# Performance work log

Measured on AMD Instinct MI355X. Metric: run time of the kernel, lower is better.

The kernel has to match this reference:

```python
import jax, jax.numpy as jnp
import numpy as np

B, S, D = 4, 2048, 1024
H = 16
HD = D // H  # 64


def setup_inputs() -> dict:
    key = jax.random.key(0)
    kx, kq, kp = jax.random.split(key, 3)
    x = jax.random.normal(kx, (B, S, D), dtype=jnp.float32)
    # torch Linear weights are [out, in]; match init scale ~ U(-1/sqrt(in), 1/sqrt(in))
    lim = 1.0 / np.sqrt(D)
    w_qkv = jax.random.uniform(kq, (3 * D, D), dtype=jnp.float32, minval=-lim, maxval=lim)
    w_proj = jax.random.uniform(kp, (D, D), dtype=jnp.float32, minval=-lim, maxval=lim)
    return {"x": x, "w_qkv": w_qkv, "w_proj": w_proj}


def reference(x, w_qkv, w_proj):
    b, s, d = x.shape
    qkv = jnp.einsum('bsd,ed->bse', x, w_qkv)  # [B,S,3D]
    q, k, v = jnp.split(qkv, 3, axis=-1)
    # [B,H,S,HD]
    q = q.reshape(b, s, H, HD).transpose(0, 2, 1, 3)
    k = k.reshape(b, s, H, HD).transpose(0, 2, 1, 3)
    v = v.reshape(b, s, H, HD).transpose(0, 2, 1, 3)
    scale = 1.0 / np.sqrt(HD)
    attn = jnp.einsum('bhqd,bhkd->bhqk', q, k) * scale  # [B,H,S,S]
    causal = jnp.tril(jnp.ones((s, s), dtype=bool))
    attn = jnp.where(causal[None, None], attn, -jnp.inf)
    attn = jax.nn.softmax(attn, axis=-1)
    out = jnp.einsum('bhqk,bhkd->bhqd', attn, v)
    out = out.transpose(0, 2, 1, 3).reshape(b, s, d)
    return jnp.einsum('bsd,ed->bse', out, w_proj)
```

## Files before the change

### kernel.cpp

```cpp
#include <hip/hip_runtime.h>

typedef unsigned short u16;
typedef unsigned int u32;

#define B_ 4
#define S_ 2048
#define D_ 1024
#define H_ 16
#define HD_ 64
#define M_ (B_ * S_)
#define QK_ (2 * D_)

typedef __bf16 bf16x8 __attribute__((ext_vector_type(8)));
typedef float f32x4 __attribute__((ext_vector_type(4)));

#define MASKVAL (-1.0e30f)
#define RESCALE_THR 8.0f

static __device__ __forceinline__ u16 f2bf_hw(float f) {
    union { __bf16 b; u16 u; } v;
    v.b = (__bf16)f;
    return v.u;
}

static __device__ __forceinline__ void gload16(const u16* g, u16* l) {
    __builtin_amdgcn_global_load_lds(
        (const __attribute__((address_space(1))) void*)g,
        (__attribute__((address_space(3))) void*)l, 16, 0, 0);
}

__global__ __launch_bounds__(256) void cvt_bf16(const float* __restrict__ src,
                                                u16* __restrict__ dst) {
    size_t i = ((size_t)blockIdx.x * 256 + threadIdx.x) * 8;
    float4 a = *(const float4*)(src + i);
    float4 b = *(const float4*)(src + i + 4);
    union { u16 h[8]; int4 v; } pk;
    pk.h[0] = f2bf_hw(a.x); pk.h[1] = f2bf_hw(a.y);
    pk.h[2] = f2bf_hw(a.z); pk.h[3] = f2bf_hw(a.w);
    pk.h[4] = f2bf_hw(b.x); pk.h[5] = f2bf_hw(b.y);
    pk.h[6] = f2bf_hw(b.z); pk.h[7] = f2bf_hw(b.w);
    *(int4*)(dst + i) = pk.v;
}

template <int EPI>
__global__ __launch_bounds__(256) void gemm_bb(const u16* __restrict__ A,
                                               const u16* __restrict__ Bw,
                                               void* __restrict__ Cout,
                                               int Ndim, int Kdim) {
    __shared__ u16 Alds[128 * 64];
    __shared__ u16 Blds[128 * 64];
    const int t = threadIdx.x;
    const int bx = blockIdx.x, by = blockIdx.y;
    const int wave = t >> 6, lane = t & 63;
    const int ml = lane & 15, quad = lane >> 4;
    const int wm = (wave >> 1) * 64, wn = (wave & 1) * 64;
    const int rowA0 = by * 128, rowB0 = bx * 128;
    const int sr8 = lane >> 3;
    const int sc8 = (lane & 7) * 8;

    f32x4 acc[4][4];
    const f32x4 zero = {0.f, 0.f, 0.f, 0.f};
#pragma unroll
    for (int i = 0; i < 4; ++i)
#pragma unroll
        for (int j = 0; j < 4; ++j) acc[i][j] = zero;

    for (int k0 = 0; k0 < Kdim; k0 += 64) {
        __syncthreads();
#pragma unroll
        for (int p = 0; p < 4; ++p) {
            const int rbase = wave * 32 + p * 8;
            gload16(&A[(size_t)(rowA0 + rbase + sr8) * Kdim + k0 + sc8],
                    &Alds[rbase * 64]);
            gload16(&Bw[(size_t)(rowB0 + rbase + sr8) * Kdim + k0 + sc8],
                    &Blds[rbase * 64]);
        }
        __syncthreads();
#pragma unroll
        for (int kc = 0; kc < 2; ++kc) {
            bf16x8 a[4], b[4];
#pragma unroll
            for (int i = 0; i < 4; ++i)
                a[i] = *(const bf16x8*)(&Alds[(wm + i * 16 + ml) * 64 + kc * 32 + quad * 8]);
#pragma unroll
            for (int j = 0; j < 4; ++j)
                b[j] = *(const bf16x8*)(&Blds[(wn + j * 16 + ml) * 64 + kc * 32 + quad * 8]);
#pragma unroll
            for (int i = 0; i < 4; ++i)
#pragma unroll
                for (int j = 0; j < 4; ++j)
                    acc[i][j] = __builtin_amdgcn_mfma_f32_16x16x32_bf16(a[i], b[j], acc[i][j], 0, 0, 0);
        }
    }

    if constexpr (EPI == 0) {
        u16* C = (u16*)Cout;
#pragma unroll
        for (int i = 0; i < 4; ++i)
#pragma unroll
            for (int j = 0; j < 4; ++j)
#pragma unroll
                for (int r = 0; r < 4; ++r) {
                    int row = rowA0 + wm + i * 16 + quad * 4 + r;
                    int col = rowB0 + wn + j * 16 + ml;
                    C[(size_t)row * Ndim + col] = f2bf_hw(acc[i][j][r]);
                }
    } else if constexpr (EPI == 1) {
        u16* Vt = (u16*)Cout;
#pragma unroll
        for (int i = 0; i < 4; ++i)
#pragma unroll
            for (int j = 0; j < 4; ++j) {
                int row0 = rowA0 + wm + i * 16 + quad * 4;
                int col = rowB0 + wn + j * 16 + ml;
                int b = row0 >> 11;
                int s0 = row0 & (S_ - 1);
                union { u16 h[4]; ushort4 v; } pk;
#pragma unroll
                for (int r = 0; r < 4; ++r) pk.h[r] = f2bf_hw(acc[i][j][r]);
                *(ushort4*)(&Vt[((size_t)(b * D_ + col)) * S_ + s0]) = pk.v;
            }
    } else {
        float* C = (float*)Cout;
#pragma unroll
        for (int i = 0; i < 4; ++i)
#pragma unroll
            for (int j = 0; j < 4; ++j)
#pragma unroll
                for (int r = 0; r < 4; ++r) {
                    int row = rowA0 + wm + i * 16 + quad * 4 + r;
                    int col = rowB0 + wn + j * 16 + ml;
                    C[(size_t)row * Ndim + col] = acc[i][j][r];
                }
    }
}

__global__ __launch_bounds__(256, 3) void attn3(const u16* __restrict__ qk,
                                                const u16* __restrict__ Vt,
                                                u16* __restrict__ AO) {
    __shared__ u16 Klds[2][64 * 64];
    __shared__ u16 Vlds[2][64 * 64];
    __shared__ u32 Pw[4][32 * 32];
    const int t = threadIdx.x;
    const int wave = t >> 6, lane = t & 63;
    const int ml = lane & 15, quad = lane >> 4;

    const int jj = blockIdx.x >> 6;
    const int bh = blockIdx.x & 63;
    const int t4 = jj >> 2, r4 = jj & 3;
    const int j = (t4 < 2) ? (15 - 4 * t4 - r4) : (12 - 4 * t4 + r4);
    const int b = bh >> 4, h = bh & 15;
    const size_t rowbase = (size_t)b * S_;

    const int srow8 = lane >> 3;
    const int schunk = ((lane & 7) ^ srow8) * 8;

    const int qj0 = j * 128 + wave * 32;
    const int ktw = 2 * j + (wave >> 1);
    const int ktmax = 2 * j + 1;

    bf16x8 qf[2][2];
#pragma unroll
    for (int mi = 0; mi < 2; ++mi)
#pragma unroll
        for (int kc = 0; kc < 2; ++kc) {
            bf16x8 q = *(const bf16x8*)(&qk[(rowbase + qj0 + mi * 16 + ml) * QK_ +
                                            h * HD_ + kc * 32 + quad * 8]);
#pragma unroll
            for (int e = 0; e < 8; ++e) {
                float f = (float)q[e] * 0.125f;
                q[e] = (__bf16)f;
            }
            qf[mi][kc] = q;
        }

    f32x4 o[2][4];
    float m[2], ls[2];
    const f32x4 zero = {0.f, 0.f, 0.f, 0.f};
#pragma unroll
    for (int mi = 0; mi < 2; ++mi) {
#pragma unroll
        for (int nd = 0; nd < 4; ++nd) o[mi][nd] = zero;
        m[mi] = MASKVAL; ls[mi] = 0.f;
    }

    auto STAGE = [&](int buf, int kt) {
        const int kb = kt * 64;
#pragma unroll
        for (int p = 0; p < 2; ++p) {
            const int rbase = wave * 16 + p * 8;
            gload16(&qk[(rowbase + kb + rbase + srow8) * QK_ + D_ + h * HD_ + schunk],
                    &Klds[buf][rbase * 64]);
            gload16(&Vt[(size_t)(bh * HD_ + rbase + srow8) * S_ + kb + schunk],
                    &Vlds[buf][rbase * 64]);
        }
    };

    STAGE(0, 0);

    for (int kt = 0; kt <= ktmax; ++kt) {
        const int cur = kt & 1;
        if (kt < ktmax) {
            STAGE(cur ^ 1, kt + 1);
            asm volatile("s_waitcnt vmcnt(4)" ::: "memory");
        } else {
            asm volatile("s_waitcnt vmcnt(0)" ::: "memory");
        }
        __builtin_amdgcn_s_barrier();

        if (kt <= ktw) {
            const int kb = kt * 64;
            bf16x8 kf[4][2], vf[4][2];
#pragma unroll
            for (int ni = 0; ni < 4; ++ni)
#pragma unroll
                for (int kc = 0; kc < 2; ++kc) {
                    const int row = ni * 16 + ml;
                    const int sw = ((kc * 4 + quad) ^ (ml & 7)) * 8;
                    kf[ni][kc] = *(const bf16x8*)(&Klds[cur][row * 64 + sw]);
                    vf[ni][kc] = *(const bf16x8*)(&Vlds[cur][row * 64 + sw]);
                }

            f32x4 sc[2][4];
            __builtin_amdgcn_s_setprio(1);
#pragma unroll
            for (int mi = 0; mi < 2; ++mi)
#pragma unroll
                for (int ni = 0; ni < 4; ++ni) {
                    f32x4 s = zero;
#pragma unroll
                    for (int kc = 0; kc < 2; ++kc)
                        s = __builtin_amdgcn_mfma_f32_16x16x32_bf16(kf[ni][kc], qf[mi][kc], s, 0, 0, 0);
                    sc[mi][ni] = s;
                }
            __builtin_amdgcn_s_setprio(0);

            if (kb + 63 > qj0) {
#pragma unroll
                for (int mi = 0; mi < 2; ++mi) {
                    const int q = qj0 + mi * 16 + ml;
#pragma unroll
                    for (int ni = 0; ni < 4; ++ni)
#pragma unroll
                        for (int r = 0; r < 4; ++r) {
                            int k = kb + ni * 16 + quad * 4 + r;
                            if (k > q) sc[mi][ni][r] = MASKVAL;
                        }
                }
            }

#pragma unroll
            for (int mi = 0; mi < 2; ++mi) {
                float tm = sc[mi][0][0];
#pragma unroll
                for (int ni = 0; ni < 4; ++ni)
#pragma unroll
                    for (int r = 0; r < 4; ++r) tm = fmaxf(tm, sc[mi][ni][r]);
                tm = fmaxf(tm, __shfl_xor(tm, 16, 64));
                tm = fmaxf(tm, __shfl_xor(tm, 32, 64));
                if (__any(tm > m[mi] + RESCALE_THR)) {
                    float mn = fmaxf(m[mi], tm);
                    float al = __expf(m[mi] - mn);
                    m[mi] = mn;
                    ls[mi] *= al;
                    float alr[4];
#pragma unroll
                    for (int r = 0; r < 4; ++r)
                        alr[r] = __shfl(al, (lane & 48) + ((lane & 48) >> 2) + r, 64);
#pragma unroll
                    for (int nd = 0; nd < 4; ++nd)
#pragma unroll
                        for (int r = 0; r < 4; ++r) o[mi][nd][r] *= alr[r];
                }
                float sum = 0.f;
#pragma unroll
                for (int ni = 0; ni < 4; ++ni)
#pragma unroll
                    for (int r = 0; r < 4; ++r) {
                        float e = __expf(sc[mi][ni][r] - m[mi]);
                        sc[mi][ni][r] = e;
                        sum += e;
                    }
                ls[mi] += sum;
#pragma unroll
                for (int ni = 0; ni < 4; ++ni) {
                    union { u16 h[4]; ushort4 v; } pk;
#pragma unroll
                    for (int r = 0; r < 4; ++r) pk.h[r] = f2bf_hw(sc[mi][ni][r]);
                    const int row = mi * 16 + ml;
                    const int word = row * 32 +
                                     (((ni * 2 + (quad >> 1)) ^ (ml & 7)) << 2) +
                                     ((quad & 1) * 2);
                    *(ushort4*)(&Pw[wave][word]) = pk.v;
                }
            }
            asm volatile("s_waitcnt lgkmcnt(0)" ::: "memory");
            bf16x8 pf[2][2];
#pragma unroll
            for (int mi = 0; mi < 2; ++mi)
#pragma unroll
                for (int kc = 0; kc < 2; ++kc) {
                    const int row = mi * 16 + ml;
                    const int word = row * 32 + ((((kc * 4 + quad)) ^ (ml & 7)) << 2);
                    pf[mi][kc] = *(const bf16x8*)(&Pw[wave][word]);
                }
            __builtin_amdgcn_s_setprio(1);
#pragma unroll
            for (int mi = 0; mi < 2; ++mi)
#pragma unroll
                for (int nd = 0; nd < 4; ++nd)
#pragma unroll
                    for (int kc = 0; kc < 2; ++kc)
                        o[mi][nd] = __builtin_amdgcn_mfma_f32_16x16x32_bf16(pf[mi][kc], vf[nd][kc],
                                                                            o[mi][nd], 0, 0, 0);
            __builtin_amdgcn_s_setprio(0);
        }
        __builtin_amdgcn_s_barrier();
    }

#pragma unroll
    for (int mi = 0; mi < 2; ++mi) {
        float s = ls[mi];
        s += __shfl_xor(s, 16, 64);
        s += __shfl_xor(s, 32, 64);
        float rl = 1.0f / s;
        float rlr[4];
#pragma unroll
        for (int r = 0; r < 4; ++r)
            rlr[r] = __shfl(rl, (lane & 48) + ((lane & 48) >> 2) + r, 64);
#pragma unroll
        for (int nd = 0; nd < 4; ++nd)
#pragma unroll
            for (int r = 0; r < 4; ++r) {
                int srow = qj0 + mi * 16 + quad * 4 + r;
                AO[(rowbase + srow) * D_ + h * HD_ + nd * 16 + ml] =
                    f2bf_hw(o[mi][nd][r] * rlr[r]);
            }
    }
}

__global__ __launch_bounds__(256) void copy16(const int4* __restrict__ src,
                                              int4* __restrict__ dst) {
    size_t i = (size_t)blockIdx.x * 256 + threadIdx.x;
    dst[i] = src[i];
}

extern "C" void kernel_launch(void* const* d_in, const int* in_sizes, int n_in,
                              void* d_out, int out_size, void* d_ws, size_t ws_size,
                              hipStream_t stream) {
    const float* x = (const float*)d_in[0];
    const float* wqkv = (const float*)d_in[1];
    const float* wproj = (const float*)d_in[2];
    float* out = (float*)d_out;

    u16* qkw = (u16*)d_ws;
    u16* Vtw = qkw + (size_t)M_ * QK_;

    u16* xb = (u16*)d_out;
    u16* wprojb = xb + (size_t)M_ * D_;
    u16* wqkvb = wprojb + (size_t)D_ * D_;

    const size_t need = ((size_t)M_ * QK_ + 8388608  + (size_t)M_ * D_  +
                         (size_t)D_ * D_ ) * sizeof(u16);
    const bool bigws = ws_size >= need;
    u16* AOb    = bigws ? (Vtw + (size_t)8388608) : xb;
    u16* wprojd = bigws ? (AOb + (size_t)M_ * D_) : wprojb;
    u16* AOp    = bigws ? AOb : qkw;
    u16* wprojp = bigws ? wprojd : qkw + (size_t)M_ * D_;

    cvt_bf16<<<dim3(M_ * D_ / 2048), 256, 0, stream>>>(x, xb);
    cvt_bf16<<<dim3(D_ * D_ / 2048), 256, 0, stream>>>(wproj, wprojd);
    cvt_bf16<<<dim3(3 * D_ * D_ / 2048), 256, 0, stream>>>(wqkv, wqkvb);

    gemm_bb<0><<<dim3(QK_ / 128, M_ / 128), 256, 0, stream>>>(xb, wqkvb, qkw, QK_, D_);
    gemm_bb<1><<<dim3(D_ / 128, M_ / 128), 256, 0, stream>>>(
        xb, wqkvb + (size_t)QK_ * D_, Vtw, D_, D_);
    attn3<<<dim3(1024), 256, 0, stream>>>(qkw, Vtw, AOb);
    if (!bigws) {
        copy16<<<dim3((unsigned)(((size_t)M_ * D_ + (size_t)D_ * D_) * 2 / (256 * 16))),
                 256, 0, stream>>>((const int4*)AOb, (int4*)qkw);
    }
    gemm_bb<2><<<dim3(D_ / 128, M_ / 128), 256, 0, stream>>>(AOp, wprojp, out, D_, D_);
}
```

Before: 269.1 us.

## Merge QK and V projection GEMMs and defer PV MFMA to overlap next tile load

The separate QK and V projection GEMMs become one launch, with the epilogue choosing row-major or transposed V output by block column. In attention, the P·V product is deferred to the next iteration so it runs after the next K/V tile load is issued, overlapping MFMA work with memory latency. The P scratch buffer changes to a padded 72-element row layout with a simpler swizzle. K fragments are now loaded per column tile to reduce register pressure. V fragments persist across iterations, which raises register use and adds a tail PV call after the loop.

```diff
diff --git a/kernel.cpp b/kernel.cpp
--- a/kernel.cpp
+++ b/kernel.cpp
@@ -46,6 +46,7 @@
 __global__ __launch_bounds__(256) void gemm_bb(const u16* __restrict__ A,
                                                const u16* __restrict__ Bw,
                                                void* __restrict__ Cout,
+                                               void* __restrict__ C2,
                                                int Ndim, int Kdim) {
     __shared__ u16 Alds[128 * 64];
     __shared__ u16 Blds[128 * 64];
@@ -93,7 +94,8 @@
         }
     }
 
-    if constexpr (EPI == 0) {
+    const bool doVt = (EPI == 1) || (EPI == 3 && bx >= 16);
+    if ((EPI == 0) || (EPI == 3 && !doVt)) {
         u16* C = (u16*)Cout;
 #pragma unroll
         for (int i = 0; i < 4; ++i)
@@ -105,14 +107,15 @@
                     int col = rowB0 + wn + j * 16 + ml;
                     C[(size_t)row * Ndim + col] = f2bf_hw(acc[i][j][r]);
                 }
-    } else if constexpr (EPI == 1) {
-        u16* Vt = (u16*)Cout;
+    } else if (doVt) {
+        u16* Vt = (EPI == 3) ? (u16*)C2 : (u16*)Cout;
+        const int voff = (EPI == 3) ? 2048 : 0;
 #pragma unroll
         for (int i = 0; i < 4; ++i)
 #pragma unroll
             for (int j = 0; j < 4; ++j) {
                 int row0 = rowA0 + wm + i * 16 + quad * 4;
-                int col = rowB0 + wn + j * 16 + ml;
+                int col = rowB0 + wn + j * 16 + ml - voff;
                 int b = row0 >> 11;
                 int s0 = row0 & (S_ - 1);
                 union { u16 h[4]; ushort4 v; } pk;
@@ -140,10 +143,11 @@
                                                 u16* __restrict__ AO) {
     __shared__ u16 Klds[2][64 * 64];
     __shared__ u16 Vlds[2][64 * 64];
-    __shared__ u32 Pw[4][32 * 32];
+    __shared__ u16 Pw[4][32 * 72];
     const int t = threadIdx.x;
     const int wave = t >> 6, lane = t & 63;
     const int ml = lane & 15, quad = lane >> 4;
+    const int mhx = (ml & 8) >> 1;
 
     const int jj = blockIdx.x >> 6;
     const int bh = blockIdx.x & 63;
@@ -159,6 +163,8 @@
     const int ktw = 2 * j + (wave >> 1);
     const int ktmax = 2 * j + 1;
 
+    u16* pwb = &Pw[wave][0];
+
     bf16x8 qf[2][2];
 #pragma unroll
     for (int mi = 0; mi < 2; ++mi)
@@ -183,6 +189,8 @@
         for (int nd = 0; nd < 4; ++nd) o[mi][nd] = zero;
         m[mi] = MASKVAL; ls[mi] = 0.f;
     }
+
+    bf16x8 vf[4][2];
 
     auto STAGE = [&](int buf, int kt) {
         const int kb = kt * 64;
@@ -196,12 +204,35 @@
         }
     };
 
+    auto PV = [&]() {
+        bf16x8 pf[2][2];
+#pragma unroll
+        for (int mi = 0; mi < 2; ++mi)
+#pragma unroll
+            for (int kc = 0; kc < 2; ++kc)
+                pf[mi][kc] = *(const bf16x8*)(&pwb[(mi * 16 + ml) * 72 +
+                                                   (((kc * 4 + quad) ^ mhx) << 3)]);
+        __builtin_amdgcn_s_setprio(1);
+#pragma unroll
+        for (int mi = 0; mi < 2; ++mi)
+#pragma unroll
+            for (int nd = 0; nd < 4; ++nd)
+#pragma unroll
+                for (int kc = 0; kc < 2; ++kc)
+                    o[mi][nd] = __builtin_amdgcn_mfma_f32_16x16x32_bf16(pf[mi][kc], vf[nd][kc],
+                                                                        o[mi][nd], 0, 0, 0);
+        __builtin_amdgcn_s_setprio(0);
+    };
+
     STAGE(0, 0);
 
     for (int kt = 0; kt <= ktmax; ++kt) {
         const int cur = kt & 1;
+        if (kt < ktmax) STAGE(cur ^ 1, kt + 1);
+
+        if (kt >= 1 && kt - 1 <= ktw) PV();
+
         if (kt < ktmax) {
-            STAGE(cur ^ 1, kt + 1);
             asm volatile("s_waitcnt vmcnt(4)" ::: "memory");
         } else {
             asm volatile("s_waitcnt vmcnt(0)" ::: "memory");
@@ -210,29 +241,19 @@
 
         if (kt <= ktw) {
             const int kb = kt * 64;
-            bf16x8 kf[4][2], vf[4][2];
-#pragma unroll
-            for (int ni = 0; ni < 4; ++ni)
-#pragma unroll
-                for (int kc = 0; kc < 2; ++kc) {
-                    const int row = ni * 16 + ml;
-                    const int sw = ((kc * 4 + quad) ^ (ml & 7)) * 8;
-                    kf[ni][kc] = *(const bf16x8*)(&Klds[cur][row * 64 + sw]);
-                    vf[ni][kc] = *(const bf16x8*)(&Vlds[cur][row * 64 + sw]);
-                }
-
             f32x4 sc[2][4];
             __builtin_amdgcn_s_setprio(1);
 #pragma unroll
-            for (int mi = 0; mi < 2; ++mi)
-#pragma unroll
-                for (int ni = 0; ni < 4; ++ni) {
-                    f32x4 s = zero;
-#pragma unroll
-                    for (int kc = 0; kc < 2; ++kc)
-                        s = __builtin_amdgcn_mfma_f32_16x16x32_bf16(kf[ni][kc], qf[mi][kc], s, 0, 0, 0);
-                    sc[mi][ni] = s;
-                }
+            for (int ni = 0; ni < 4; ++ni) {
+                const int row = ni * 16 + ml;
+                bf16x8 kfa = *(const bf16x8*)(&Klds[cur][row * 64 + ((quad ^ (ml & 7)) << 3)]);
+                bf16x8 kfb = *(const bf16x8*)(&Klds[cur][row * 64 + (((4 + quad) ^ (ml & 7)) << 3)]);
+#pragma unroll
+                for (int mi = 0; mi < 2; ++mi) {
+                    f32x4 s = __builtin_amdgcn_mfma_f32_16x16x32_bf16(kfa, qf[mi][0], zero, 0, 0, 0);
+                    sc[mi][ni] = __builtin_amdgcn_mfma_f32_16x16x32_bf16(kfb, qf[mi][1], s, 0, 0, 0);
+                }
+            }
             __builtin_amdgcn_s_setprio(0);
 
             if (kb + 63 > qj0) {
@@ -287,36 +308,25 @@
                     union { u16 h[4]; ushort4 v; } pk;
 #pragma unroll
                     for (int r = 0; r < 4; ++r) pk.h[r] = f2bf_hw(sc[mi][ni][r]);
-                    const int row = mi * 16 + ml;
-                    const int word = row * 32 +
-                                     (((ni * 2 + (quad >> 1)) ^ (ml & 7)) << 2) +
-                                     ((quad & 1) * 2);
-                    *(ushort4*)(&Pw[wave][word]) = pk.v;
-                }
-            }
-            asm volatile("s_waitcnt lgkmcnt(0)" ::: "memory");
-            bf16x8 pf[2][2];
-#pragma unroll
-            for (int mi = 0; mi < 2; ++mi)
-#pragma unroll
-                for (int kc = 0; kc < 2; ++kc) {
-                    const int row = mi * 16 + ml;
-                    const int word = row * 32 + ((((kc * 4 + quad)) ^ (ml & 7)) << 2);
-                    pf[mi][kc] = *(const bf16x8*)(&Pw[wave][word]);
-                }
-            __builtin_amdgcn_s_setprio(1);
-#pragma unroll
-            for (int mi = 0; mi < 2; ++mi)
-#pragma unroll
-                for (int nd = 0; nd < 4; ++nd)
-#pragma unroll
-                    for (int kc = 0; kc < 2; ++kc)
-                        o[mi][nd] = __builtin_amdgcn_mfma_f32_16x16x32_bf16(pf[mi][kc], vf[nd][kc],
-                                                                            o[mi][nd], 0, 0, 0);
-            __builtin_amdgcn_s_setprio(0);
-        }
+                    const int off = (mi * 16 + ml) * 72 +
+                                    ((((2 * ni + (quad >> 1)) ^ mhx)) << 3) + ((quad & 1) << 2);
+                    *(ushort4*)(&pwb[off]) = pk.v;
+                }
+            }
+#pragma unroll
+            for (int ni = 0; ni < 4; ++ni) {
+                const int row = ni * 16 + ml;
+#pragma unroll
+                for (int kc = 0; kc < 2; ++kc)
+                    vf[ni][kc] = *(const bf16x8*)(&Vlds[cur][row * 64 +
+                                                            (((kc * 4 + quad) ^ (ml & 7)) << 3)]);
+            }
+        }
+        asm volatile("s_waitcnt lgkmcnt(0)" ::: "memory");
         __builtin_amdgcn_s_barrier();
     }
+
+    if (ktw == ktmax) PV();
 
 #pragma unroll
     for (int mi = 0; mi < 2; ++mi) {
@@ -372,13 +382,13 @@
     cvt_bf16<<<dim3(D_ * D_ / 2048), 256, 0, stream>>>(wproj, wprojd);
     cvt_bf16<<<dim3(3 * D_ * D_ / 2048), 256, 0, stream>>>(wqkv, wqkvb);
 
-    gemm_bb<0><<<dim3(QK_ / 128, M_ / 128), 256, 0, stream>>>(xb, wqkvb, qkw, QK_, D_);
-    gemm_bb<1><<<dim3(D_ / 128, M_ / 128), 256, 0, stream>>>(
-        xb, wqkvb + (size_t)QK_ * D_, Vtw, D_, D_);
+    gemm_bb<3><<<dim3(3 * D_ / 128, M_ / 128), 256, 0, stream>>>(
+        xb, wqkvb, qkw, Vtw, QK_, D_);
     attn3<<<dim3(1024), 256, 0, stream>>>(qkw, Vtw, AOb);
     if (!bigws) {
         copy16<<<dim3((unsigned)(((size_t)M_ * D_ + (size_t)D_ * D_) * 2 / (256 * 16))),
                  256, 0, stream>>>((const int4*)AOb, (int4*)qkw);
     }
-    gemm_bb<2><<<dim3(D_ / 128, M_ / 128), 256, 0, stream>>>(AOp, wprojp, out, D_, D_);
-}
+    gemm_bb<2><<<dim3(D_ / 128, M_ / 128), 256, 0, stream>>>(
+        AOp, wprojp, out, nullptr, D_, D_);
+}
```

Result: no change. 266.7 us (-0.9%).
